# Kernel optimization log

Measured on AMD Instinct MI355X. Metric: run time of the kernel, lower is better.

## Reference

```python
import jax, jax.numpy as jnp
import numpy as np

HIDDEN = 3584
NUM_HEADS = 28
NUM_KV_HEADS = 4
HEAD_DIM = 128
ROPE_THETA = 1000000.0


def setup_inputs() -> dict:
    key = jax.random.key(0)
    ks = jax.random.split(key, 12)
    B, S, C = 2, 1024, 3072
    inp = {
        "positions": jnp.arange(B * S, dtype=jnp.int32).reshape(B, S),
        "hidden_states": jax.random.normal(ks[0], (B, S, HIDDEN), dtype=jnp.float32),
        "k_cache": jax.random.normal(ks[1], (B, NUM_KV_HEADS, C, HEAD_DIM), dtype=jnp.float32),
        "v_cache": jax.random.normal(ks[2], (B, NUM_KV_HEADS, C, HEAD_DIM), dtype=jnp.float32),
        "cache_len": C,
        # torch Linear weights are [out_features, in_features]
        "q_w": jax.random.normal(ks[3], (NUM_HEADS * HEAD_DIM, HIDDEN), dtype=jnp.float32) * 0.02,
        "q_b": jax.random.normal(ks[4], (NUM_HEADS * HEAD_DIM,), dtype=jnp.float32) * 0.02,
        "k_w": jax.random.normal(ks[5], (NUM_KV_HEADS * HEAD_DIM, HIDDEN), dtype=jnp.float32) * 0.02,
        "k_b": jax.random.normal(ks[6], (NUM_KV_HEADS * HEAD_DIM,), dtype=jnp.float32) * 0.02,
        "v_w": jax.random.normal(ks[7], (NUM_KV_HEADS * HEAD_DIM, HIDDEN), dtype=jnp.float32) * 0.02,
        "v_b": jax.random.normal(ks[8], (NUM_KV_HEADS * HEAD_DIM,), dtype=jnp.float32) * 0.02,
        "o_w": jax.random.normal(ks[9], (HIDDEN, NUM_HEADS * HEAD_DIM), dtype=jnp.float32) * 0.02,
    }
    return inp


def _rope_cos_sin(positions, head_dim, base):
    # positions: [B,S] -> cos/sin [B,1,S,head_dim]
    inv_freq = 1.0 / (base ** (jnp.arange(0, head_dim, 2, dtype=jnp.float32) / head_dim))
    freqs = positions.astype(jnp.float32)[..., None] * inv_freq  # [B,S,D/2]
    emb = jnp.concatenate([freqs, freqs], axis=-1)               # [B,S,D]
    return jnp.cos(emb)[:, None], jnp.sin(emb)[:, None]


def _rotate_half(x):
    d = x.shape[-1] // 2
    return jnp.concatenate([-x[..., d:], x[..., :d]], axis=-1)


def reference(positions, hidden_states, k_cache, v_cache, cache_len,
              q_w, q_b, k_w, k_b, v_w, v_b, o_w):
    B, S, _ = hidden_states.shape
    scale = HEAD_DIM ** -0.5

    # QKV projections -> [B, H, S, D]
    q = (hidden_states @ q_w.T + q_b).reshape(B, S, NUM_HEADS, HEAD_DIM).transpose(0, 2, 1, 3)
    k = (hidden_states @ k_w.T + k_b).reshape(B, S, NUM_KV_HEADS, HEAD_DIM).transpose(0, 2, 1, 3)
    v = (hidden_states @ v_w.T + v_b).reshape(B, S, NUM_KV_HEADS, HEAD_DIM).transpose(0, 2, 1, 3)

    cos, sin = _rope_cos_sin(positions, HEAD_DIM, ROPE_THETA)
    q = q * cos + _rotate_half(q) * sin
    k = k * cos + _rotate_half(k) * sin

    # KV-cache concat (cache_len is static == full cache length here)
    k_full = jnp.concatenate([k_cache[:, :, :cache_len], k], axis=2)
    v_full = jnp.concatenate([v_cache[:, :, :cache_len], v], axis=2)
    new_k, new_v = k_full, v_full

    # GQA repeat: [B, Hkv, T, D] -> [B, H, T, D]
    groups = NUM_HEADS // NUM_KV_HEADS
    k_rep = jnp.repeat(k_full, groups, axis=1)
    v_rep = jnp.repeat(v_full, groups, axis=1)

    # Non-causal SDPA
    scores = jnp.einsum('bhqd,bhkd->bhqk', q, k_rep) * scale
    probs = jax.nn.softmax(scores, axis=-1)
    attn = jnp.einsum('bhqk,bhkd->bhqd', probs, v_rep)

    attn = attn.transpose(0, 2, 1, 3).reshape(B, S, NUM_HEADS * HEAD_DIM)
    out = attn @ o_w.T
    return out, new_k, new_v
```

## Files before the change

kernel.cpp:

```cpp
#include <hip/hip_runtime.h>
#include <hip/hip_bf16.h>
#include <math.h>

#define HIDDEN 3584
#define NHEADS 28
#define NKV 4
#define HDIM 128
#define BB 2
#define SS 1024
#define CC 3072
#define TT 4096
#define BS 2048
#define NQ 3584
#define GROUPS 7
#define SCALE 0.08838834764831845f
#define NT (HIDDEN / 32)
#define SM_OFF 16.0f

typedef unsigned short u16;
typedef __attribute__((ext_vector_type(4))) unsigned short u16x4;
typedef __attribute__((ext_vector_type(8))) unsigned short u16x8;
typedef __attribute__((ext_vector_type(8))) short s16x8;
typedef __attribute__((ext_vector_type(4))) float f32x4;

__device__ inline u16 f2bf(float x) {
  union { float f; unsigned int u; } v; v.f = x;
  unsigned int r = v.u + 0x7FFFu + ((v.u >> 16) & 1u);
  return (u16)(r >> 16);
}
__device__ inline unsigned int cvtpk(float lo, float hi) {
  unsigned int r;
  asm("v_cvt_pk_bf16_f32 %0, %1, %2" : "=v"(r) : "v"(lo), "v"(hi));
  return r;
}

__global__ __launch_bounds__(256) void copy_cache_kernel(
    const float4* __restrict__ kc, const float4* __restrict__ vc,
    float4* __restrict__ nk, float4* __restrict__ nv,
    u16* __restrict__ kbf, u16* __restrict__ vbft) {
  __shared__ u16 Tr[128][72];
  const int bh = blockIdx.y;
  const int t0 = blockIdx.x * 64;
  const int tid = threadIdx.x;
  #pragma unroll
  for (int i = 0; i < 8; ++i) {
    int idx = i * 256 + tid;
    int r = idx >> 5, c = idx & 31;
    size_t src = ((size_t)bh * CC + t0 + r) * 32 + c;
    size_t dst = ((size_t)bh * TT + t0 + r) * 32 + c;
    float4 k4 = kc[src], v4 = vc[src];
    nk[dst] = k4; nv[dst] = v4;
    u16x4 kb; kb[0] = f2bf(k4.x); kb[1] = f2bf(k4.y); kb[2] = f2bf(k4.z); kb[3] = f2bf(k4.w);
    *(u16x4*)(kbf + dst * 4) = kb;
    Tr[c * 4 + 0][r] = f2bf(v4.x);
    Tr[c * 4 + 1][r] = f2bf(v4.y);
    Tr[c * 4 + 2][r] = f2bf(v4.z);
    Tr[c * 4 + 3][r] = f2bf(v4.w);
  }
  __syncthreads();
  const int d = tid >> 1, half = tid & 1;
  const size_t obase = ((size_t)bh * 128 + d) * (size_t)TT + t0 + half * 32;
  #pragma unroll
  for (int i = 0; i < 4; ++i) {
    u16x8 v = *(const u16x8*)&Tr[d][half * 32 + i * 8];
    *(u16x8*)(vbft + obase + i * 8) = v;
  }
}

__global__ __launch_bounds__(256) void cvt_bf16_kernel(
    const float4* __restrict__ src, u16* __restrict__ dst, int n4) {
  int i = blockIdx.x * 256 + threadIdx.x;
  if (i < n4) {
    float4 v = src[i];
    u16x4 o; o[0] = f2bf(v.x); o[1] = f2bf(v.y); o[2] = f2bf(v.z); o[3] = f2bf(v.w);
    *(u16x4*)(dst + (size_t)i * 4) = o;
  }
}

__global__ __launch_bounds__(256) void gemm_qkv_kernel(
    const u16* __restrict__ hbf,
    const float* __restrict__ qw, const float* __restrict__ qb,
    const float* __restrict__ kw, const float* __restrict__ kb,
    const float* __restrict__ vw, const float* __restrict__ vb,
    const int* __restrict__ pos,
    u16* __restrict__ qbf, float* __restrict__ nk, float* __restrict__ nv,
    u16* __restrict__ kbf, u16* __restrict__ vbft) {
  __shared__ u16 Ab[2][128 * 32];
  __shared__ u16 Bb[2][128 * 32];
  const int tid = threadIdx.x;
  const int w = tid >> 6, lane = tid & 63, lr = lane & 15, lg = lane >> 4;
  const int m0 = blockIdx.y * 128, n0 = blockIdx.x * 128;

  const bool isq = (n0 < NQ);
  const bool isk = (!isq) && (n0 < NQ + 512);
  const float* Wb; const float* bias;
  if (isq)      { Wb = qw + (size_t)n0 * HIDDEN;          bias = qb + n0; }
  else if (isk) { Wb = kw + (size_t)(n0 - NQ) * HIDDEN;   bias = kb + (n0 - NQ); }
  else          { Wb = vw + (size_t)(n0 - NQ - 512) * HIDDEN; bias = vb + (n0 - NQ - 512); }

  f32x4 acc[2][8];
  #pragma unroll
  for (int f = 0; f < 2; ++f)
    #pragma unroll
    for (int n = 0; n < 8; ++n) acc[f][n] = (f32x4){0.f, 0.f, 0.f, 0.f};

  const int br = tid >> 1, bkh = (tid & 1) * 16;
  const float* Bsrc = Wb + (size_t)br * HIDDEN + bkh;

  auto stageA = [&](int buf, int k0) {
    #pragma unroll
    for (int i = 0; i < 2; ++i) {
      int ci = w * 128 + i * 64 + lane;
      int row = ci >> 2, c = ci & 3;
      __builtin_amdgcn_global_load_lds(
          (const __attribute__((address_space(1))) void*)(hbf + (size_t)(m0 + row) * HIDDEN + k0 + c * 8),
          (__attribute__((address_space(3))) void*)(&Ab[buf][(w * 128 + i * 64) * 8]),
          16, 0, 0);
    }
  };

  float4 fB[4];
  auto loadB = [&](int k0) {
    #pragma unroll
    for (int j = 0; j < 4; ++j) fB[j] = *(const float4*)(Bsrc + k0 + j * 4);
  };
  auto writeB = [&](int buf) {
    unsigned int pk[8];
    pk[0] = cvtpk(fB[0].x, fB[0].y); pk[1] = cvtpk(fB[0].z, fB[0].w);
    pk[2] = cvtpk(fB[1].x, fB[1].y); pk[3] = cvtpk(fB[1].z, fB[1].w);
    pk[4] = cvtpk(fB[2].x, fB[2].y); pk[5] = cvtpk(fB[2].z, fB[2].w);
    pk[6] = cvtpk(fB[3].x, fB[3].y); pk[7] = cvtpk(fB[3].z, fB[3].w);
    *(uint4*)&Bb[buf][br * 32 + bkh]     = make_uint4(pk[0], pk[1], pk[2], pk[3]);
    *(uint4*)&Bb[buf][br * 32 + bkh + 8] = make_uint4(pk[4], pk[5], pk[6], pk[7]);
  };

  stageA(0, 0);
  loadB(0);
  writeB(0);
  __syncthreads();

  for (int kt = 0; kt < NT; ++kt) {
    const int cur = kt & 1;
    if (kt + 1 < NT) {
      stageA(cur ^ 1, (kt + 1) * 32);
      loadB((kt + 1) * 32);
    }
    s16x8 af[2];
    af[0] = *(const s16x8*)&Ab[cur][(w * 32 + lr) * 32 + lg * 8];
    af[1] = *(const s16x8*)&Ab[cur][(w * 32 + 16 + lr) * 32 + lg * 8];
    #pragma unroll
    for (int n = 0; n < 8; ++n) {
      const s16x8 bf_ = *(const s16x8*)&Bb[cur][(n * 16 + lr) * 32 + lg * 8];
      acc[0][n] = __builtin_amdgcn_mfma_f32_16x16x32_bf16(af[0], bf_, acc[0][n], 0, 0, 0);
      acc[1][n] = __builtin_amdgcn_mfma_f32_16x16x32_bf16(af[1], bf_, acc[1][n], 0, 0, 0);
    }
    if (kt + 1 < NT) writeB(cur ^ 1);
    __syncthreads();
  }

  float bias_v[8];
  #pragma unroll
  for (int n = 0; n < 8; ++n) bias_v[n] = bias[n * 16 + lr];
  float invf[4];
  if (isq || isk) {
    #pragma unroll
    for (int n = 0; n < 4; ++n)
      invf[n] = __expf(-(float)(n * 16 + lr) * 0.21586735246819178f);
  }
  const int kvh = isq ? 0 : ((isk ? (n0 - NQ) : (n0 - NQ - 512)) >> 7);

  #pragma unroll
  for (int f = 0; f < 2; ++f)
    #pragma unroll
    for (int reg = 0; reg < 4; ++reg) {
      int m = m0 + w * 32 + f * 16 + lg * 4 + reg;
      float y[8];
      #pragma unroll
      for (int n = 0; n < 8; ++n) y[n] = acc[f][n][reg] + bias_v[n];
      if (isq || isk) {
        float p = (float)pos[m];
        #pragma unroll
        for (int n = 0; n < 4; ++n) {
          float sA, cA;
          __sincosf(p * invf[n], &sA, &cA);
          float lo = y[n], hi = y[n + 4];
          y[n]     = lo * cA - hi * sA;
          y[n + 4] = hi * cA + lo * sA;
        }
      }
      if (isq) {
        u16* dst = qbf + (size_t)m * NQ + n0;
        #pragma unroll
        for (int n = 0; n < 8; ++n) dst[n * 16 + lr] = f2bf(y[n] * SCALE);
      } else {
        int b_ = m >> 10, s_ = m & 1023;
        size_t rowoff = ((size_t)(b_ * NKV + kvh) * TT + CC + s_) * HDIM;
        if (isk) {
          #pragma unroll
          for (int n = 0; n < 8; ++n) {
            nk[rowoff + n * 16 + lr]  = y[n];
            kbf[rowoff + n * 16 + lr] = f2bf(y[n]);
          }
        } else {
          size_t vb0 = (size_t)(b_ * NKV + kvh) * 128;
          #pragma unroll
          for (int n = 0; n < 8; ++n) {
            nv[rowoff + n * 16 + lr] = y[n];
            vbft[(vb0 + n * 16 + lr) * (size_t)TT + CC + s_] = f2bf(y[n]);
          }
        }
      }
    }
}

__global__ __launch_bounds__(256) void gemm_out_kernel(
    const u16* __restrict__ Abf, const float* __restrict__ W,
    float* __restrict__ Y) {
  __shared__ u16 Ab[2][128 * 32];
  __shared__ u16 Bb[2][128 * 32];
  const int tid = threadIdx.x;
  const int w = tid >> 6, lane = tid & 63, lr = lane & 15, lg = lane >> 4;
  const int m0 = blockIdx.y * 128, n0 = blockIdx.x * 128;

  f32x4 acc[2][8];
  #pragma unroll
  for (int f = 0; f < 2; ++f)
    #pragma unroll
    for (int n = 0; n < 8; ++n) acc[f][n] = (f32x4){0.f, 0.f, 0.f, 0.f};

  const int br = tid >> 1, bkh = (tid & 1) * 16;
  const float* Bsrc = W + (size_t)(n0 + br) * HIDDEN + bkh;

  auto stageA = [&](int buf, int k0) {
    #pragma unroll
    for (int i = 0; i < 2; ++i) {
      int ci = w * 128 + i * 64 + lane;
      int row = ci >> 2, c = ci & 3;
      __builtin_amdgcn_global_load_lds(
          (const __attribute__((address_space(1))) void*)(Abf + (size_t)(m0 + row) * HIDDEN + k0 + c * 8),
          (__attribute__((address_space(3))) void*)(&Ab[buf][(w * 128 + i * 64) * 8]),
          16, 0, 0);
    }
  };

  float4 fB[4];
  auto loadB = [&](int k0) {
    #pragma unroll
    for (int j = 0; j < 4; ++j) fB[j] = *(const float4*)(Bsrc + k0 + j * 4);
  };
  auto writeB = [&](int buf) {
    unsigned int pk[8];
    pk[0] = cvtpk(fB[0].x, fB[0].y); pk[1] = cvtpk(fB[0].z, fB[0].w);
    pk[2] = cvtpk(fB[1].x, fB[1].y); pk[3] = cvtpk(fB[1].z, fB[1].w);
    pk[4] = cvtpk(fB[2].x, fB[2].y); pk[5] = cvtpk(fB[2].z, fB[2].w);
    pk[6] = cvtpk(fB[3].x, fB[3].y); pk[7] = cvtpk(fB[3].z, fB[3].w);
    *(uint4*)&Bb[buf][br * 32 + bkh]     = make_uint4(pk[0], pk[1], pk[2], pk[3]);
    *(uint4*)&Bb[buf][br * 32 + bkh + 8] = make_uint4(pk[4], pk[5], pk[6], pk[7]);
  };

  stageA(0, 0);
  loadB(0);
  writeB(0);
  __syncthreads();

  for (int kt = 0; kt < NT; ++kt) {
    const int cur = kt & 1;
    if (kt + 1 < NT) {
      stageA(cur ^ 1, (kt + 1) * 32);
      loadB((kt + 1) * 32);
    }
    s16x8 af[2];
    af[0] = *(const s16x8*)&Ab[cur][(w * 32 + lr) * 32 + lg * 8];
    af[1] = *(const s16x8*)&Ab[cur][(w * 32 + 16 + lr) * 32 + lg * 8];
    #pragma unroll
    for (int n = 0; n < 8; ++n) {
      const s16x8 bf_ = *(const s16x8*)&Bb[cur][(n * 16 + lr) * 32 + lg * 8];
      acc[0][n] = __builtin_amdgcn_mfma_f32_16x16x32_bf16(af[0], bf_, acc[0][n], 0, 0, 0);
      acc[1][n] = __builtin_amdgcn_mfma_f32_16x16x32_bf16(af[1], bf_, acc[1][n], 0, 0, 0);
    }
    if (kt + 1 < NT) writeB(cur ^ 1);
    __syncthreads();
  }

  #pragma unroll
  for (int f = 0; f < 2; ++f)
    #pragma unroll
    for (int reg = 0; reg < 4; ++reg) {
      int m = m0 + w * 32 + f * 16 + lg * 4 + reg;
      float* dst = Y + (size_t)m * NQ + n0;
      #pragma unroll
      for (int n = 0; n < 8; ++n) dst[n * 16 + lr] = acc[f][n][reg];
    }
}

__global__ __launch_bounds__(512, 2) void attn_kernel(
    const u16* __restrict__ qbf, const u16* __restrict__ kbf,
    const u16* __restrict__ vbft, u16* __restrict__ aout) {
  __shared__ __align__(16) u16 SMEM[53248];

  const int orig = blockIdx.x;
  const int swzb = (orig & 7) * 28 + (orig >> 3);
  const int g    = swzb / 28;
  const int ii   = swzb % 28;
  const int b    = g >> 2;
  const int hkv  = g & 3;
  const int h    = hkv * GROUPS + (ii >> 2);
  const int q0   = (ii & 3) * 256;

  const int tid  = threadIdx.x;
  const int w    = tid >> 6;
  const int quad = w >> 2;
  const int wq   = w & 3;
  const int lane = tid & 63;
  const int lr   = lane & 15;
  const int lg   = lane >> 4;
  const int qw0  = q0 + wq * 64;

  s16x8 qf[4][4];
  #pragma unroll
  for (int fq = 0; fq < 4; ++fq) {
    const u16* qp = qbf + (size_t)(b * SS + qw0 + fq * 16 + lr) * NQ + h * HDIM + lg * 8;
    #pragma unroll
    for (int kk = 0; kk < 4; ++kk) qf[fq][kk] = *(const s16x8*)(qp + kk * 32);
  }

  const size_t bh = (size_t)(b * NKV + hkv);
  const u16* kB = kbf  + bh * (size_t)TT * HDIM;
  const u16* vB = vbft + bh * (size_t)HDIM * TT;

  f32x4 oacc[4][8];
  #pragma unroll
  for (int fq = 0; fq < 4; ++fq)
    #pragma unroll
    for (int n = 0; n < 8; ++n) oacc[fq][n] = (f32x4){0.f, 0.f, 0.f, 0.f};
  float lsum[4] = {0.f, 0.f, 0.f, 0.f};

  u16* Ksq = SMEM + quad * 8192;
  u16* Vsq = SMEM + 16384 + quad * 8192;
  u16* Psw = SMEM + 32768 + w * 2560;

  auto stage = [&](int buf, int kt) {
    #pragma unroll
    for (int i = 0; i < 2; ++i) {
      int ci = (wq * 2 + i) * 64 + lane;
      int krow = ci >> 4, kc_ = ci & 15;
      const u16* ksrc = kB + (size_t)(kt * 32 + krow) * HDIM + ((kc_ ^ (krow & 7)) * 8);
      __builtin_amdgcn_global_load_lds(
          (const __attribute__((address_space(1))) void*)ksrc,
          (__attribute__((address_space(3))) void*)(Ksq + buf * 4096 + (wq * 2 + i) * 512),
          16, 0, 0);
      int vd = ci >> 2, vc_ = ci & 3;
      const u16* vsrc = vB + (size_t)vd * TT + kt * 32 + vc_ * 8;
      __builtin_amdgcn_global_load_lds(
          (const __attribute__((address_space(1))) void*)vsrc,
          (__attribute__((address_space(3))) void*)(Vsq + buf * 4096 + (wq * 2 + i) * 512),
          16, 0, 0);
    }
  };

  const int tbase = quad * 64;
  stage(0, tbase);
  __syncthreads();

  for (int it = 0; it < 64; ++it) {
    const int cur = it & 1;
    if (it + 1 < 64) stage(cur ^ 1, tbase + it + 1);

    f32x4 sacc[4][2];
    #pragma unroll
    for (int fq = 0; fq < 4; ++fq)
      #pragma unroll
      for (int n = 0; n < 2; ++n) sacc[fq][n] = (f32x4){0.f, 0.f, 0.f, 0.f};
    __builtin_amdgcn_s_setprio(1);
    #pragma unroll
    for (int kk = 0; kk < 4; ++kk) {
      #pragma unroll
      for (int n = 0; n < 2; ++n) {
        int row = n * 16 + lr;
        const s16x8 kf = *(const s16x8*)&Ksq[cur * 4096 + row * 128 + (((kk * 4 + lg) ^ (row & 7)) * 8)];
        #pragma unroll
        for (int fq = 0; fq < 4; ++fq)
          sacc[fq][n] = __builtin_amdgcn_mfma_f32_16x16x32_bf16(kf, qf[fq][kk], sacc[fq][n], 0, 0, 0);
      }
    }
    __builtin_amdgcn_s_setprio(0);

    #pragma unroll
    for (int fq = 0; fq < 4; ++fq) {
      #pragma unroll
      for (int n = 0; n < 2; ++n) {
        float p0 = __expf(sacc[fq][n][0] - SM_OFF);
        float p1 = __expf(sacc[fq][n][1] - SM_OFF);
        float p2 = __expf(sacc[fq][n][2] - SM_OFF);
        float p3 = __expf(sacc[fq][n][3] - SM_OFF);
        lsum[fq] += (p0 + p1) + (p2 + p3);
        uint2 pk = make_uint2(cvtpk(p0, p1), cvtpk(p2, p3));
        *(uint2*)&Psw[fq * 640 + lr * 40 + n * 16 + lg * 4] = pk;
      }
    }

    s16x8 pa[4];
    #pragma unroll
    for (int fq = 0; fq < 4; ++fq)
      pa[fq] = *(const s16x8*)&Psw[fq * 640 + lr * 40 + lg * 8];
    __builtin_amdgcn_s_setprio(1);
    #pragma unroll
    for (int n = 0; n < 8; ++n) {
      int row = n * 16 + lr;
      const s16x8 vf = *(const s16x8*)&Vsq[cur * 4096 + row * 32 + lg * 8];
      #pragma unroll
      for (int fq = 0; fq < 4; ++fq)
        oacc[fq][n] = __builtin_amdgcn_mfma_f32_16x16x32_bf16(pa[fq], vf, oacc[fq][n], 0, 0, 0);
    }
    __builtin_amdgcn_s_setprio(0);

    __syncthreads();
  }

  f32x4* OX = (f32x4*)SMEM;
  float* LX = (float*)(SMEM + 32768);
  #pragma unroll
  for (int half = 0; half < 2; ++half) {
    if (quad == 1) {
      #pragma unroll
      for (int fp = 0; fp < 2; ++fp) {
        int fq = half * 2 + fp;
        #pragma unroll
        for (int n = 0; n < 8; ++n)
          OX[(fp * 8 + n) * 256 + wq * 64 + lane] = oacc[fq][n];
      }
      if (half == 0) {
        #pragma unroll
        for (int fq = 0; fq < 4; ++fq) LX[fq * 256 + wq * 64 + lane] = lsum[fq];
      }
    }
    __syncthreads();
    if (quad == 0) {
      #pragma unroll
      for (int fp = 0; fp < 2; ++fp) {
        int fq = half * 2 + fp;
        #pragma unroll
        for (int n = 0; n < 8; ++n) {
          f32x4 v = OX[(fp * 8 + n) * 256 + wq * 64 + lane];
          oacc[fq][n] += v;
        }
      }
      if (half == 0) {
        #pragma unroll
        for (int fq = 0; fq < 4; ++fq) lsum[fq] += LX[fq * 256 + wq * 64 + lane];
      }
    }
    __syncthreads();
  }

  if (quad == 0) {
    #pragma unroll
    for (int fq = 0; fq < 4; ++fq) {
      float s = lsum[fq];
      s += __shfl_xor(s, 16);
      s += __shfl_xor(s, 32);
      #pragma unroll
      for (int reg = 0; reg < 4; ++reg) {
        int qrow = lg * 4 + reg;
        float invl = 1.f / __shfl(s, qrow);
        u16* orow = aout + (size_t)(b * SS + qw0 + fq * 16 + qrow) * NQ + h * HDIM;
        #pragma unroll
        for (int n = 0; n < 8; ++n)
          orow[n * 16 + lr] = f2bf(oacc[fq][n][reg] * invl);
      }
    }
  }
}

extern "C" void kernel_launch(void* const* d_in, const int* in_sizes, int n_in,
                              void* d_out, int out_size, void* d_ws, size_t ws_size,
                              hipStream_t stream) {
  const int*   positions = (const int*)d_in[0];
  const float* hidden    = (const float*)d_in[1];
  const float* kcache    = (const float*)d_in[2];
  const float* vcache    = (const float*)d_in[3];
  const float* qw = (const float*)d_in[5];
  const float* qb = (const float*)d_in[6];
  const float* kw = (const float*)d_in[7];
  const float* kb = (const float*)d_in[8];
  const float* vw = (const float*)d_in[9];
  const float* vb = (const float*)d_in[10];
  const float* ow = (const float*)d_in[11];

  float* out = (float*)d_out;
  float* nk  = out + (size_t)BS * NQ;
  float* nv  = nk + (size_t)BB * NKV * TT * HDIM;

  u16* qbf  = (u16*)d_ws;
  u16* kbf  = qbf + (size_t)BS * NQ;
  u16* vbft = kbf + (size_t)BB * NKV * TT * HDIM;
  u16* hbf  = vbft + (size_t)BB * NKV * HDIM * TT;
  u16* aws  = hbf;

  copy_cache_kernel<<<dim3(CC / 64, BB * NKV), 256, 0, stream>>>(
      (const float4*)kcache, (const float4*)vcache,
      (float4*)nk, (float4*)nv, kbf, vbft);
  cvt_bf16_kernel<<<(BS * HIDDEN / 4 + 255) / 256, 256, 0, stream>>>(
      (const float4*)hidden, hbf, BS * HIDDEN / 4);
  gemm_qkv_kernel<<<dim3(36, 16), 256, 0, stream>>>(
      hbf, qw, qb, kw, kb, vw, vb, positions, qbf, nk, nv, kbf, vbft);
  attn_kernel<<<224, 512, 0, stream>>>(qbf, kbf, vbft, aws);
  gemm_out_kernel<<<dim3(28, 16), 256, 0, stream>>>(aws, ow, out);
}
```

Measured before the change: 453.2 us.

## Pre-convert projection weights to bf16 and stage both GEMM operands via direct LDS loads

After: 405.2 us. 10.6% less time.

```diff
diff --git a/kernel.cpp b/kernel.cpp
--- a/kernel.cpp
+++ b/kernel.cpp
@@ -77,12 +77,11 @@
   }
 }
 
-__global__ __launch_bounds__(256) void gemm_qkv_kernel(
-    const u16* __restrict__ hbf,
-    const float* __restrict__ qw, const float* __restrict__ qb,
-    const float* __restrict__ kw, const float* __restrict__ kb,
-    const float* __restrict__ vw, const float* __restrict__ vb,
-    const int* __restrict__ pos,
+
+__global__ __launch_bounds__(256) void gemm_qkv_bf_kernel(
+    const u16* __restrict__ hbf, const u16* __restrict__ wbf,
+    const float* __restrict__ qb, const float* __restrict__ kb,
+    const float* __restrict__ vb, const int* __restrict__ pos,
     u16* __restrict__ qbf, float* __restrict__ nk, float* __restrict__ nv,
     u16* __restrict__ kbf, u16* __restrict__ vbft) {
   __shared__ u16 Ab[2][128 * 32];
@@ -93,10 +92,10 @@
 
   const bool isq = (n0 < NQ);
   const bool isk = (!isq) && (n0 < NQ + 512);
-  const float* Wb; const float* bias;
-  if (isq)      { Wb = qw + (size_t)n0 * HIDDEN;          bias = qb + n0; }
-  else if (isk) { Wb = kw + (size_t)(n0 - NQ) * HIDDEN;   bias = kb + (n0 - NQ); }
-  else          { Wb = vw + (size_t)(n0 - NQ - 512) * HIDDEN; bias = vb + (n0 - NQ - 512); }
+  const float* bias;
+  if (isq)      bias = qb + n0;
+  else if (isk) bias = kb + (n0 - NQ);
+  else          bias = vb + (n0 - NQ - 512);
 
   f32x4 acc[2][8];
   #pragma unroll
@@ -104,10 +103,7 @@
     #pragma unroll
     for (int n = 0; n < 8; ++n) acc[f][n] = (f32x4){0.f, 0.f, 0.f, 0.f};
 
-  const int br = tid >> 1, bkh = (tid & 1) * 16;
-  const float* Bsrc = Wb + (size_t)br * HIDDEN + bkh;
-
-  auto stageA = [&](int buf, int k0) {
+  auto stageAB = [&](int buf, int k0) {
     #pragma unroll
     for (int i = 0; i < 2; ++i) {
       int ci = w * 128 + i * 64 + lane;
@@ -116,35 +112,19 @@
           (const __attribute__((address_space(1))) void*)(hbf + (size_t)(m0 + row) * HIDDEN + k0 + c * 8),
           (__attribute__((address_space(3))) void*)(&Ab[buf][(w * 128 + i * 64) * 8]),
           16, 0, 0);
-    }
-  };
-
-  float4 fB[4];
-  auto loadB = [&](int k0) {
-    #pragma unroll
-    for (int j = 0; j < 4; ++j) fB[j] = *(const float4*)(Bsrc + k0 + j * 4);
-  };
-  auto writeB = [&](int buf) {
-    unsigned int pk[8];
-    pk[0] = cvtpk(fB[0].x, fB[0].y); pk[1] = cvtpk(fB[0].z, fB[0].w);
-    pk[2] = cvtpk(fB[1].x, fB[1].y); pk[3] = cvtpk(fB[1].z, fB[1].w);
-    pk[4] = cvtpk(fB[2].x, fB[2].y); pk[5] = cvtpk(fB[2].z, fB[2].w);
-    pk[6] = cvtpk(fB[3].x, fB[3].y); pk[7] = cvtpk(fB[3].z, fB[3].w);
-    *(uint4*)&Bb[buf][br * 32 + bkh]     = make_uint4(pk[0], pk[1], pk[2], pk[3]);
-    *(uint4*)&Bb[buf][br * 32 + bkh + 8] = make_uint4(pk[4], pk[5], pk[6], pk[7]);
-  };
-
-  stageA(0, 0);
-  loadB(0);
-  writeB(0);
+      __builtin_amdgcn_global_load_lds(
+          (const __attribute__((address_space(1))) void*)(wbf + (size_t)(n0 + row) * HIDDEN + k0 + c * 8),
+          (__attribute__((address_space(3))) void*)(&Bb[buf][(w * 128 + i * 64) * 8]),
+          16, 0, 0);
+    }
+  };
+
+  stageAB(0, 0);
   __syncthreads();
 
   for (int kt = 0; kt < NT; ++kt) {
     const int cur = kt & 1;
-    if (kt + 1 < NT) {
-      stageA(cur ^ 1, (kt + 1) * 32);
-      loadB((kt + 1) * 32);
-    }
+    if (kt + 1 < NT) stageAB(cur ^ 1, (kt + 1) * 32);
     s16x8 af[2];
     af[0] = *(const s16x8*)&Ab[cur][(w * 32 + lr) * 32 + lg * 8];
     af[1] = *(const s16x8*)&Ab[cur][(w * 32 + 16 + lr) * 32 + lg * 8];
@@ -154,7 +134,6 @@
       acc[0][n] = __builtin_amdgcn_mfma_f32_16x16x32_bf16(af[0], bf_, acc[0][n], 0, 0, 0);
       acc[1][n] = __builtin_amdgcn_mfma_f32_16x16x32_bf16(af[1], bf_, acc[1][n], 0, 0, 0);
     }
-    if (kt + 1 < NT) writeB(cur ^ 1);
     __syncthreads();
   }
 
@@ -213,6 +192,197 @@
     }
 }
 
+__global__ __launch_bounds__(256) void gemm_out_bf_kernel(
+    const u16* __restrict__ Abf, const u16* __restrict__ Wbf,
+    float* __restrict__ Y) {
+  __shared__ u16 Ab[2][128 * 32];
+  __shared__ u16 Bb[2][128 * 32];
+  const int tid = threadIdx.x;
+  const int w = tid >> 6, lane = tid & 63, lr = lane & 15, lg = lane >> 4;
+  const int m0 = blockIdx.y * 128, n0 = blockIdx.x * 128;
+
+  f32x4 acc[2][8];
+  #pragma unroll
+  for (int f = 0; f < 2; ++f)
+    #pragma unroll
+    for (int n = 0; n < 8; ++n) acc[f][n] = (f32x4){0.f, 0.f, 0.f, 0.f};
+
+  auto stageAB = [&](int buf, int k0) {
+    #pragma unroll
+    for (int i = 0; i < 2; ++i) {
+      int ci = w * 128 + i * 64 + lane;
+      int row = ci >> 2, c = ci & 3;
+      __builtin_amdgcn_global_load_lds(
+          (const __attribute__((address_space(1))) void*)(Abf + (size_t)(m0 + row) * HIDDEN + k0 + c * 8),
+          (__attribute__((address_space(3))) void*)(&Ab[buf][(w * 128 + i * 64) * 8]),
+          16, 0, 0);
+      __builtin_amdgcn_global_load_lds(
+          (const __attribute__((address_space(1))) void*)(Wbf + (size_t)(n0 + row) * HIDDEN + k0 + c * 8),
+          (__attribute__((address_space(3))) void*)(&Bb[buf][(w * 128 + i * 64) * 8]),
+          16, 0, 0);
+    }
+  };
+
+  stageAB(0, 0);
+  __syncthreads();
+
+  for (int kt = 0; kt < NT; ++kt) {
+    const int cur = kt & 1;
+    if (kt + 1 < NT) stageAB(cur ^ 1, (kt + 1) * 32);
+    s16x8 af[2];
+    af[0] = *(const s16x8*)&Ab[cur][(w * 32 + lr) * 32 + lg * 8];
+    af[1] = *(const s16x8*)&Ab[cur][(w * 32 + 16 + lr) * 32 + lg * 8];
+    #pragma unroll
+    for (int n = 0; n < 8; ++n) {
+      const s16x8 bf_ = *(const s16x8*)&Bb[cur][(n * 16 + lr) * 32 + lg * 8];
+      acc[0][n] = __builtin_amdgcn_mfma_f32_16x16x32_bf16(af[0], bf_, acc[0][n], 0, 0, 0);
+      acc[1][n] = __builtin_amdgcn_mfma_f32_16x16x32_bf16(af[1], bf_, acc[1][n], 0, 0, 0);
+    }
+    __syncthreads();
+  }
+
+  #pragma unroll
+  for (int f = 0; f < 2; ++f)
+    #pragma unroll
+    for (int reg = 0; reg < 4; ++reg) {
+      int m = m0 + w * 32 + f * 16 + lg * 4 + reg;
+      float* dst = Y + (size_t)m * NQ + n0;
+      #pragma unroll
+      for (int n = 0; n < 8; ++n) dst[n * 16 + lr] = acc[f][n][reg];
+    }
+}
+
+__global__ __launch_bounds__(256) void gemm_qkv_kernel(
+    const u16* __restrict__ hbf,
+    const float* __restrict__ qw, const float* __restrict__ qb,
+    const float* __restrict__ kw, const float* __restrict__ kb,
+    const float* __restrict__ vw, const float* __restrict__ vb,
+    const int* __restrict__ pos,
+    u16* __restrict__ qbf, float* __restrict__ nk, float* __restrict__ nv,
+    u16* __restrict__ kbf, u16* __restrict__ vbft) {
+  __shared__ u16 Ab[2][128 * 32];
+  __shared__ u16 Bb[2][128 * 32];
+  const int tid = threadIdx.x;
+  const int w = tid >> 6, lane = tid & 63, lr = lane & 15, lg = lane >> 4;
+  const int m0 = blockIdx.y * 128, n0 = blockIdx.x * 128;
+
+  const bool isq = (n0 < NQ);
+  const bool isk = (!isq) && (n0 < NQ + 512);
+  const float* Wb; const float* bias;
+  if (isq)      { Wb = qw + (size_t)n0 * HIDDEN;          bias = qb + n0; }
+  else if (isk) { Wb = kw + (size_t)(n0 - NQ) * HIDDEN;   bias = kb + (n0 - NQ); }
+  else          { Wb = vw + (size_t)(n0 - NQ - 512) * HIDDEN; bias = vb + (n0 - NQ - 512); }
+
+  f32x4 acc[2][8];
+  #pragma unroll
+  for (int f = 0; f < 2; ++f)
+    #pragma unroll
+    for (int n = 0; n < 8; ++n) acc[f][n] = (f32x4){0.f, 0.f, 0.f, 0.f};
+
+  const int br = tid >> 1, bkh = (tid & 1) * 16;
+  const float* Bsrc = Wb + (size_t)br * HIDDEN + bkh;
+
+  auto stageA = [&](int buf, int k0) {
+    #pragma unroll
+    for (int i = 0; i < 2; ++i) {
+      int ci = w * 128 + i * 64 + lane;
+      int row = ci >> 2, c = ci & 3;
+      __builtin_amdgcn_global_load_lds(
+          (const __attribute__((address_space(1))) void*)(hbf + (size_t)(m0 + row) * HIDDEN + k0 + c * 8),
+          (__attribute__((address_space(3))) void*)(&Ab[buf][(w * 128 + i * 64) * 8]),
+          16, 0, 0);
+    }
+  };
+
+  float4 fB[4];
+  auto loadB = [&](int k0) {
+    #pragma unroll
+    for (int j = 0; j < 4; ++j) fB[j] = *(const float4*)(Bsrc + k0 + j * 4);
+  };
+  auto writeB = [&](int buf) {
+    unsigned int pk[8];
+    pk[0] = cvtpk(fB[0].x, fB[0].y); pk[1] = cvtpk(fB[0].z, fB[0].w);
+    pk[2] = cvtpk(fB[1].x, fB[1].y); pk[3] = cvtpk(fB[1].z, fB[1].w);
+    pk[4] = cvtpk(fB[2].x, fB[2].y); pk[5] = cvtpk(fB[2].z, fB[2].w);
+    pk[6] = cvtpk(fB[3].x, fB[3].y); pk[7] = cvtpk(fB[3].z, fB[3].w);
+    *(uint4*)&Bb[buf][br * 32 + bkh]     = make_uint4(pk[0], pk[1], pk[2], pk[3]);
+    *(uint4*)&Bb[buf][br * 32 + bkh + 8] = make_uint4(pk[4], pk[5], pk[6], pk[7]);
+  };
+
+  stageA(0, 0); loadB(0); writeB(0);
+  __syncthreads();
+
+  for (int kt = 0; kt < NT; ++kt) {
+    const int cur = kt & 1;
+    if (kt + 1 < NT) { stageA(cur ^ 1, (kt + 1) * 32); loadB((kt + 1) * 32); }
+    s16x8 af[2];
+    af[0] = *(const s16x8*)&Ab[cur][(w * 32 + lr) * 32 + lg * 8];
+    af[1] = *(const s16x8*)&Ab[cur][(w * 32 + 16 + lr) * 32 + lg * 8];
+    #pragma unroll
+    for (int n = 0; n < 8; ++n) {
+      const s16x8 bf_ = *(const s16x8*)&Bb[cur][(n * 16 + lr) * 32 + lg * 8];
+      acc[0][n] = __builtin_amdgcn_mfma_f32_16x16x32_bf16(af[0], bf_, acc[0][n], 0, 0, 0);
+      acc[1][n] = __builtin_amdgcn_mfma_f32_16x16x32_bf16(af[1], bf_, acc[1][n], 0, 0, 0);
+    }
+    if (kt + 1 < NT) writeB(cur ^ 1);
+    __syncthreads();
+  }
+
+  float bias_v[8];
+  #pragma unroll
+  for (int n = 0; n < 8; ++n) bias_v[n] = bias[n * 16 + lr];
+  float invf[4];
+  if (isq || isk) {
+    #pragma unroll
+    for (int n = 0; n < 4; ++n)
+      invf[n] = __expf(-(float)(n * 16 + lr) * 0.21586735246819178f);
+  }
+  const int kvh = isq ? 0 : ((isk ? (n0 - NQ) : (n0 - NQ - 512)) >> 7);
+
+  #pragma unroll
+  for (int f = 0; f < 2; ++f)
+    #pragma unroll
+    for (int reg = 0; reg < 4; ++reg) {
+      int m = m0 + w * 32 + f * 16 + lg * 4 + reg;
+      float y[8];
+      #pragma unroll
+      for (int n = 0; n < 8; ++n) y[n] = acc[f][n][reg] + bias_v[n];
+      if (isq || isk) {
+        float p = (float)pos[m];
+        #pragma unroll
+        for (int n = 0; n < 4; ++n) {
+          float sA, cA;
+          __sincosf(p * invf[n], &sA, &cA);
+          float lo = y[n], hi = y[n + 4];
+          y[n]     = lo * cA - hi * sA;
+          y[n + 4] = hi * cA + lo * sA;
+        }
+      }
+      if (isq) {
+        u16* dst = qbf + (size_t)m * NQ + n0;
+        #pragma unroll
+        for (int n = 0; n < 8; ++n) dst[n * 16 + lr] = f2bf(y[n] * SCALE);
+      } else {
+        int b_ = m >> 10, s_ = m & 1023;
+        size_t rowoff = ((size_t)(b_ * NKV + kvh) * TT + CC + s_) * HDIM;
+        if (isk) {
+          #pragma unroll
+          for (int n = 0; n < 8; ++n) {
+            nk[rowoff + n * 16 + lr]  = y[n];
+            kbf[rowoff + n * 16 + lr] = f2bf(y[n]);
+          }
+        } else {
+          size_t vb0 = (size_t)(b_ * NKV + kvh) * 128;
+          #pragma unroll
+          for (int n = 0; n < 8; ++n) {
+            nv[rowoff + n * 16 + lr] = y[n];
+            vbft[(vb0 + n * 16 + lr) * (size_t)TT + CC + s_] = f2bf(y[n]);
+          }
+        }
+      }
+    }
+}
+
 __global__ __launch_bounds__(256) void gemm_out_kernel(
     const u16* __restrict__ Abf, const float* __restrict__ W,
     float* __restrict__ Y) {
@@ -258,17 +428,12 @@
     *(uint4*)&Bb[buf][br * 32 + bkh + 8] = make_uint4(pk[4], pk[5], pk[6], pk[7]);
   };
 
-  stageA(0, 0);
-  loadB(0);
-  writeB(0);
+  stageA(0, 0); loadB(0); writeB(0);
   __syncthreads();
 
   for (int kt = 0; kt < NT; ++kt) {
     const int cur = kt & 1;
-    if (kt + 1 < NT) {
-      stageA(cur ^ 1, (kt + 1) * 32);
-      loadB((kt + 1) * 32);
-    }
+    if (kt + 1 < NT) { stageA(cur ^ 1, (kt + 1) * 32); loadB((kt + 1) * 32); }
     s16x8 af[2];
     af[0] = *(const s16x8*)&Ab[cur][(w * 32 + lr) * 32 + lg * 8];
     af[1] = *(const s16x8*)&Ab[cur][(w * 32 + 16 + lr) * 32 + lg * 8];
@@ -297,7 +462,6 @@
     const u16* __restrict__ qbf, const u16* __restrict__ kbf,
     const u16* __restrict__ vbft, u16* __restrict__ aout) {
   __shared__ __align__(16) u16 SMEM[53248];
-
   const int orig = blockIdx.x;
   const int swzb = (orig & 7) * 28 + (orig >> 3);
   const int g    = swzb / 28;
@@ -496,14 +660,36 @@
   u16* vbft = kbf + (size_t)BB * NKV * TT * HDIM;
   u16* hbf  = vbft + (size_t)BB * NKV * HDIM * TT;
   u16* aws  = hbf;
+  u16* wqkv = hbf + (size_t)BS * NQ;
+  u16* owbf = wqkv;
+
+  const size_t fast_need = ((size_t)BS * NQ * 2 + (size_t)BB * NKV * TT * HDIM * 2
+                            + (size_t)(NQ + 1024) * HIDDEN) * sizeof(u16);
+  const bool fast = ws_size >= fast_need;
 
   copy_cache_kernel<<<dim3(CC / 64, BB * NKV), 256, 0, stream>>>(
       (const float4*)kcache, (const float4*)vcache,
       (float4*)nk, (float4*)nv, kbf, vbft);
   cvt_bf16_kernel<<<(BS * HIDDEN / 4 + 255) / 256, 256, 0, stream>>>(
       (const float4*)hidden, hbf, BS * HIDDEN / 4);
-  gemm_qkv_kernel<<<dim3(36, 16), 256, 0, stream>>>(
-      hbf, qw, qb, kw, kb, vw, vb, positions, qbf, nk, nv, kbf, vbft);
-  attn_kernel<<<224, 512, 0, stream>>>(qbf, kbf, vbft, aws);
-  gemm_out_kernel<<<dim3(28, 16), 256, 0, stream>>>(aws, ow, out);
-}
+
+  if (fast) {
+    cvt_bf16_kernel<<<(NQ * HIDDEN / 4 + 255) / 256, 256, 0, stream>>>(
+        (const float4*)qw, wqkv, NQ * HIDDEN / 4);
+    cvt_bf16_kernel<<<(512 * HIDDEN / 4 + 255) / 256, 256, 0, stream>>>(
+        (const float4*)kw, wqkv + (size_t)NQ * HIDDEN, 512 * HIDDEN / 4);
+    cvt_bf16_kernel<<<(512 * HIDDEN / 4 + 255) / 256, 256, 0, stream>>>(
+        (const float4*)vw, wqkv + (size_t)(NQ + 512) * HIDDEN, 512 * HIDDEN / 4);
+    gemm_qkv_bf_kernel<<<dim3(36, 16), 256, 0, stream>>>(
+        hbf, wqkv, qb, kb, vb, positions, qbf, nk, nv, kbf, vbft);
+    cvt_bf16_kernel<<<(NQ * HIDDEN / 4 + 255) / 256, 256, 0, stream>>>(
+        (const float4*)ow, owbf, NQ * HIDDEN / 4);
+    attn_kernel<<<224, 512, 0, stream>>>(qbf, kbf, vbft, aws);
+    gemm_out_bf_kernel<<<dim3(28, 16), 256, 0, stream>>>(aws, owbf, out);
+  } else {
+    gemm_qkv_kernel<<<dim3(36, 16), 256, 0, stream>>>(
+        hbf, qw, qb, kw, kb, vw, vb, positions, qbf, nk, nv, kbf, vbft);
+    attn_kernel<<<224, 512, 0, stream>>>(qbf, kbf, vbft, aws);
+    gemm_out_kernel<<<dim3(28, 16), 256, 0, stream>>>(aws, ow, out);
+  }
+}
```
